# Kernel optimization log

Measured on AMD Instinct MI355X. Metric: run time of the kernel, lower is better.

## Reference

```python
import jax, jax.numpy as jnp
import numpy as np

L = 28          # num_hidden_layers (kv_cache leading dim = 2*L = 56)
H = 1024        # hidden_size
NH = 8          # num_attention_heads
KVH = 4         # num_key_value_heads
HD = 128        # head_dim
I = 3072        # mlp intermediate size
VC = 4096       # codec vocab size
NCG = 16        # num_code_groups
B = 4
S = 512         # cached seq len
THETA = 1000000.0
EPS = 1e-6


def rmsnorm(x, w):
    v = jnp.mean(jnp.square(x.astype(jnp.float32)), axis=-1, keepdims=True)
    return (x * jax.lax.rsqrt(v + EPS)).astype(x.dtype) * w


def rotate_half(x):
    h = x.shape[-1] // 2
    return jnp.concatenate([-x[..., h:], x[..., :h]], axis=-1)


def setup_inputs() -> dict:
    key = jax.random.key(0)
    ks = jax.random.split(key, 16)
    def f(k, shp, s=0.02):
        return jax.random.normal(k, shp, jnp.float32) * s
    return {
        "cb0_id": jax.random.randint(ks[0], (B, 1), 0, VC),
        "cb1_15_ids": jax.random.randint(ks[1], (B, NCG - 1), 0, VC),
        "trailing_text_embed": f(ks[2], (B, 1, H), 1.0),
        "kv_cache": f(ks[3], (2 * L, B, KVH, S, HD), 1.0),
        "position": jnp.full((B,), S, dtype=jnp.int32),
        "cb0_emb": f(ks[4], (VC, H), 1.0),
        "cp_emb": f(ks[5], (NCG - 1, VC, H), 1.0),
        "Wq": f(ks[6], (L, H, NH * HD)),
        "Wk": f(ks[7], (L, H, KVH * HD)),
        "Wv": f(ks[8], (L, H, KVH * HD)),
        "Wo": f(ks[9], (L, NH * HD, H)),
        "q_norm_w": jnp.ones((L, HD), jnp.float32),
        "k_norm_w": jnp.ones((L, HD), jnp.float32),
        "ln1_w": jnp.ones((L, H), jnp.float32),
        "ln2_w": jnp.ones((L, H), jnp.float32),
        "Wgate": f(ks[10], (L, H, I)),
        "Wup": f(ks[11], (L, H, I)),
        "Wdown": f(ks[12], (L, I, H)),
        "norm_w": jnp.ones((H,), jnp.float32),
        "head_w": f(ks[13], (H, VC)),
    }


def reference(cb0_id, cb1_15_ids, trailing_text_embed, kv_cache, position,
              cb0_emb, cp_emb, Wq, Wk, Wv, Wo, q_norm_w, k_norm_w,
              ln1_w, ln2_w, Wgate, Wup, Wdown, norm_w, head_w):
    n_rep = NH // KVH
    scale = 1.0 / np.sqrt(HD).astype(np.float32)

    # --- codebook embedding sum ---
    e = cb0_emb[cb0_id[:, 0]]                                   # [B,H]
    cp = cp_emb[jnp.arange(NCG - 1)[None, :], cb1_15_ids]       # [B,15,H]
    h = (e + cp.sum(axis=1))[:, None, :] + trailing_text_embed  # [B,1,H]

    # --- rotary at current position; broadcast shape [B,1,1,HD] ---
    inv_freq = 1.0 / (THETA ** (jnp.arange(0, HD, 2, dtype=jnp.float32) / HD))
    freqs = position.astype(jnp.float32)[:, None] * inv_freq[None, :]  # [B,HD/2]
    emb = jnp.concatenate([freqs, freqs], axis=-1)              # [B,HD]
    cos = jnp.cos(emb)[:, None, None, :]
    sin = jnp.sin(emb)[:, None, None, :]

    kv = kv_cache.reshape(L, 2, B, KVH, S, HD)

    def layer(hs, xs):
        wq, wk, wv, wo, qn, kn, l1, l2, wg, wu, wd, kc, vc = xs
        x = rmsnorm(hs, l1)
        q = (x @ wq).reshape(B, 1, NH, HD)
        k = (x @ wk).reshape(B, 1, KVH, HD)
        v = (x @ wv).reshape(B, 1, KVH, HD)
        q = jnp.transpose(rmsnorm(q, qn), (0, 2, 1, 3))   # [B,NH,1,HD]
        k = jnp.transpose(rmsnorm(k, kn), (0, 2, 1, 3))   # [B,KVH,1,HD]
        v = jnp.transpose(v, (0, 2, 1, 3))
        q = q * cos + rotate_half(q) * sin
        k = k * cos + rotate_half(k) * sin
        fk = jnp.concatenate([kc, k], axis=2)             # [B,KVH,S+1,HD]
        fv = jnp.concatenate([vc, v], axis=2)
        # GQA: head h attends kv head h // n_rep == reshape grouping (q_len = 1)
        qg = q.reshape(B, KVH, n_rep, HD)
        scores = jnp.einsum('bgrd,bgsd->bgrs', qg, fk) * scale
        w = jax.nn.softmax(scores.astype(jnp.float32), axis=-1).astype(q.dtype)
        o = jnp.einsum('bgrs,bgsd->bgrd', w, fv).reshape(B, 1, NH * HD)
        hs = hs + o @ wo
        x = rmsnorm(hs, l2)
        hs = hs + (jax.nn.silu(x @ wg) * (x @ wu)) @ wd
        return hs, (k, v)

    xs = (Wq, Wk, Wv, Wo, q_norm_w, k_norm_w, ln1_w, ln2_w,
          Wgate, Wup, Wdown, kv[:, 0], kv[:, 1])
    h, (new_k, new_v) = jax.lax.scan(layer, h, xs)

    h = rmsnorm(h, norm_w)
    past_hidden = h                                       # [B,1,H]
    logits = (h @ head_w)[:, 0, :]                        # [B,VC]

    full_k = jnp.concatenate([kv[:, 0], new_k], axis=3)   # [L,B,KVH,S+1,HD]
    full_v = jnp.concatenate([kv[:, 1], new_v], axis=3)
    new_kv_cache = jnp.stack([full_k, full_v], axis=1).reshape(2 * L, B, KVH, S + 1, HD)
    return logits, new_kv_cache, past_hidden
```

## Files before the change

kernel.cpp:

```cpp
#include <hip/hip_runtime.h>
#include <math.h>

#define L_  28
#define H_  1024
#define NH_ 8
#define KVH_ 4
#define HD_ 128
#define I_  3072
#define VC_ 4096
#define B_  4
#define S_  512
#define EPS_ 1e-6f

#define WS_H     0
#define WS_SSQ1  4096
#define WS_SSQ2  4128
#define WS_QKVP  4160
#define WS_ATTO  266304
#define WS_ATML  331840
#define WS_OPP   332864
#define WS_GUP   463936
#define WS_DWP   1250368
#define WS_HDP   1446976

__device__ __forceinline__ float wave_reduce_sum(float v) {
    #pragma unroll
    for (int off = 32; off; off >>= 1) v += __shfl_down(v, off);
    return v;
}
__device__ __forceinline__ float wave_reduce_max(float v) {
    #pragma unroll
    for (int off = 32; off; off >>= 1) v = fmaxf(v, __shfl_down(v, off));
    return v;
}

__global__ __launch_bounds__(128) void k_embed(
    const int* __restrict__ cb0, const int* __restrict__ cb1,
    const float* __restrict__ trail, const float* __restrict__ cb0e,
    const float* __restrict__ cpe, float* __restrict__ h,
    float* __restrict__ ssq1)
{
    __shared__ float red[2];
    const int t = threadIdx.x;
    const int b = blockIdx.x >> 3, sl = blockIdx.x & 7;
    const int i = sl * 128 + t;
    float v = cb0e[(size_t)cb0[b] * 1024 + i] + trail[b * 1024 + i];
    #pragma unroll
    for (int j = 0; j < 15; j++)
        v += cpe[((size_t)j * 4096 + cb1[b * 15 + j]) * 1024 + i];
    h[b * 1024 + i] = v;
    float s = wave_reduce_sum(v * v);
    if ((t & 63) == 0) red[t >> 6] = s;
    __syncthreads();
    if (t == 0) ssq1[sl * 4 + b] = red[0] + red[1];
}

template<int P>
__global__ __launch_bounds__(256) void k_norm(
    const float* __restrict__ part, float* __restrict__ h,
    float* __restrict__ ssqp)
{
    __shared__ float red[2][128];
    __shared__ float r2[2];
    const int t = threadIdx.x;
    const int b = blockIdx.x >> 3, sl = blockIdx.x & 7;
    const int col = sl * 128 + (t & 127), half = t >> 7;
    float acc = 0.f;
    #pragma unroll 8
    for (int c = half * (P / 2); c < (half + 1) * (P / 2); c++)
        acc += part[(size_t)(c * 4 + b) * 1024 + col];
    red[half][t & 127] = acc;
    __syncthreads();
    if (half == 0) {
        float v = h[b * 1024 + col] + red[0][t] + red[1][t];
        h[b * 1024 + col] = v;
        float s = wave_reduce_sum(v * v);
        if ((t & 63) == 0) r2[t >> 6] = s;
    }
    __syncthreads();
    if (t == 0) ssqp[sl * 4 + b] = r2[0] + r2[1];
}

template<int RPW, int NTOT, typename F>
__device__ __forceinline__ void gemv_core(
    const float* __restrict__ W, int ldw, int wcol0, int k0,
    float* __restrict__ xsl, float4* __restrict__ accbuf,
    float* __restrict__ pp, int colblk, int ks, F&& prologue)
{
    const int t = threadIdx.x;
    const int wv = t >> 6, lane = t & 63;
    const float* Wp = W + (size_t)(k0 + wv * RPW) * ldw + wcol0 + lane * 4;
    float4 wreg[RPW];
    #pragma unroll
    for (int i = 0; i < RPW; i++) wreg[i] = *(const float4*)(Wp + (size_t)i * ldw);
    prologue();
    const float4* xs4 = (const float4*)xsl;
    float4 a0 = {0,0,0,0}, a1 = {0,0,0,0}, a2 = {0,0,0,0}, a3 = {0,0,0,0};
    #pragma unroll
    for (int i = 0; i < RPW; i++) {
        float4 w4 = wreg[i];
        float4 xb = xs4[wv * RPW + i];
        a0.x += w4.x * xb.x; a0.y += w4.y * xb.x; a0.z += w4.z * xb.x; a0.w += w4.w * xb.x;
        a1.x += w4.x * xb.y; a1.y += w4.y * xb.y; a1.z += w4.z * xb.y; a1.w += w4.w * xb.y;
        a2.x += w4.x * xb.z; a2.y += w4.y * xb.z; a2.z += w4.z * xb.z; a2.w += w4.w * xb.z;
        a3.x += w4.x * xb.w; a3.y += w4.y * xb.w; a3.z += w4.z * xb.w; a3.w += w4.w * xb.w;
    }
    accbuf[(wv * 64 + lane) * 4 + 0] = a0;
    accbuf[(wv * 64 + lane) * 4 + 1] = a1;
    accbuf[(wv * 64 + lane) * 4 + 2] = a2;
    accbuf[(wv * 64 + lane) * 4 + 3] = a3;
    __syncthreads();
    const int l2 = t >> 2, b2 = t & 3;
    float4 s0 = accbuf[(0 * 64 + l2) * 4 + b2];
    float4 s1 = accbuf[(1 * 64 + l2) * 4 + b2];
    float4 s2 = accbuf[(2 * 64 + l2) * 4 + b2];
    float4 s3 = accbuf[(3 * 64 + l2) * 4 + b2];
    float4 s;
    s.x = s0.x + s1.x + s2.x + s3.x;
    s.y = s0.y + s1.y + s2.y + s3.y;
    s.z = s0.z + s1.z + s2.z + s3.z;
    s.w = s0.w + s1.w + s2.w + s3.w;
    *(float4*)(pp + ((size_t)ks * 4 + b2) * NTOT + colblk * 256 + l2 * 4) = s;
}

__global__ __launch_bounds__(256) void k_qkv(
    const float* __restrict__ h, const float* __restrict__ ssq1,
    const float* __restrict__ ln1,
    const float* __restrict__ Wq, const float* __restrict__ Wk,
    const float* __restrict__ Wv, float* __restrict__ qkvp)
{
    __shared__ float xsl[128];
    __shared__ float4 accbuf[1024];
    const int t = threadIdx.x;
    const int ks = blockIdx.y, k0 = ks * 32, cb = blockIdx.x;
    const float* W; int ldw, wcol0;
    if (cb < 4)      { W = Wq; ldw = 1024; wcol0 = cb * 256; }
    else if (cb < 6) { W = Wk; ldw = 512;  wcol0 = (cb - 4) * 256; }
    else             { W = Wv; ldw = 512;  wcol0 = (cb - 6) * 256; }
    gemv_core<8, 2048>(W, ldw, wcol0, k0, xsl, accbuf, qkvp, cb, ks, [&]() {
        if (t < 128) {
            const int kk = t & 31, b = t >> 5;
            float ssq = 0.f;
            #pragma unroll
            for (int i = 0; i < 8; i++) ssq += ssq1[i * 4 + b];
            const float rms = rsqrtf(ssq * (1.f / 1024.f) + EPS_);
            xsl[kk * 4 + b] = h[b * 1024 + k0 + kk] * rms * ln1[k0 + kk];
        }
        __syncthreads();
    });
}

__global__ __launch_bounds__(256) void k_attn(
    const float* __restrict__ qkvp,
    const float* __restrict__ qnw, const float* __restrict__ knw,
    const float* __restrict__ kin, const float* __restrict__ vin,
    float* __restrict__ kout, float* __restrict__ vout,
    const int* __restrict__ pos,
    float* __restrict__ opart, float* __restrict__ mlpart)
{
    __shared__ float Kl[33][129];
    __shared__ float Vl[33][129];
    __shared__ float ql[2][128];
    __shared__ float sc[2][36];
    __shared__ float red[8];

    const int t = threadIdx.x;
    const int bg = blockIdx.x, b = bg >> 2, g = bg & 3;
    const int c = blockIdx.y;
    const int lane = t & 63;
    const int r = t >> 7, d = t & 127;
    const float scale = 0.088388347648318447f;

    const float posf = (float)pos[b];
    const int j = d & 63;
    const float invf = exp2f(-(float)j * 0.31143075889569021f);
    const float ang = posf * invf;
    const float cs = cosf(ang), sn = sinf(ang);
    const int pd = (d < 64) ? d + 64 : d - 64;

    float qraw = 0.f;
    {
        const int n = (2 * g + r) * 128 + d;
        #pragma unroll
        for (int cc = 0; cc < 32; cc++) qraw += qkvp[((size_t)cc * 4 + b) * 2048 + n];
    }
    ql[r][d] = qraw;
    float ssq = wave_reduce_sum(qraw * qraw);
    if (lane == 0) red[t >> 6] = ssq;
    __syncthreads();
    const float rms_q = rsqrtf((red[r * 2] + red[r * 2 + 1]) * (1.f / 128.f) + EPS_);
    float qv = qraw * rms_q * qnw[d];
    float qp = ql[r][pd] * rms_q * qnw[pd];
    float qro = qv * cs + ((d < 64) ? -qp : qp) * sn;

    float kvraw = 0.f;
    if (c == 15) {
        const int base = (t < 128) ? (1024 + g * 128 + d) : (1536 + g * 128 + d);
        #pragma unroll
        for (int cc = 0; cc < 32; cc++) kvraw += qkvp[((size_t)cc * 4 + b) * 2048 + base];
    }
    float kss = wave_reduce_sum((t < 128) ? kvraw * kvraw : 0.f);
    __syncthreads();
    ql[r][d] = qro;
    if (lane == 0 && t < 128) red[t >> 6] = kss;
    if (c == 15) { if (t < 128) Kl[32][d] = kvraw; else Vl[32][d] = kvraw; }
    __syncthreads();
    float newkv = 0.f;
    if (c == 15) {
        if (t < 128) {
            const float rms_k = rsqrtf((red[0] + red[1]) * (1.f / 128.f) + EPS_);
            float kv_ = Kl[32][d] * rms_k * knw[d];
            float kp  = Kl[32][pd] * rms_k * knw[pd];
            newkv = kv_ * cs + ((d < 64) ? -kp : kp) * sn;
        } else {
            newkv = Vl[32][d];
        }
    }
    __syncthreads();
    const size_t out_bg = (size_t)bg * (513 * 128);
    if (c == 15) {
        if (t < 128) { Kl[32][d] = newkv; kout[out_bg + 512 * 128 + d] = newkv; }
        else         { Vl[32][d] = newkv; vout[out_bg + 512 * 128 + d] = newkv; }
    }

    const size_t in_bg = (size_t)bg * (512 * 128);
    const int s0 = c * 32;
    #pragma unroll
    for (int i = 0; i < 4; i++) {
        int f4 = i * 256 + t;
        int row = f4 >> 5, d0 = (f4 & 31) * 4;
        float4 k4 = *(const float4*)(kin + in_bg + (size_t)(s0 + row) * 128 + d0);
        float4 v4 = *(const float4*)(vin + in_bg + (size_t)(s0 + row) * 128 + d0);
        Kl[row][d0] = k4.x; Kl[row][d0 + 1] = k4.y; Kl[row][d0 + 2] = k4.z; Kl[row][d0 + 3] = k4.w;
        Vl[row][d0] = v4.x; Vl[row][d0 + 1] = v4.y; Vl[row][d0 + 2] = v4.z; Vl[row][d0 + 3] = v4.w;
        *(float4*)(kout + out_bg + (size_t)(s0 + row) * 128 + d0) = k4;
        *(float4*)(vout + out_bg + (size_t)(s0 + row) * 128 + d0) = v4;
    }
    __syncthreads();

    const int nk = (c == 15) ? 33 : 32;
    const int si = d;
    float sv = -1e30f;
    if (si < nk) {
        float a = 0.f;
        #pragma unroll 8
        for (int dd = 0; dd < 128; dd++) a += ql[r][dd] * Kl[si][dd];
        sv = a * scale;
    }
    float mv = wave_reduce_max(sv);
    if (lane == 0) red[t >> 6] = mv;
    __syncthreads();
    const float m = fmaxf(red[r * 2], red[r * 2 + 1]);
    float p = (si < nk) ? expf(sv - m) : 0.f;
    if (si < nk) sc[r][si] = p;
    float lsum = wave_reduce_sum(p);
    __syncthreads();
    if (lane == 0) red[t >> 6] = lsum;
    __syncthreads();
    const float lr = red[r * 2] + red[r * 2 + 1];
    if (d == 0) {
        mlpart[(size_t)((bg * 2 + r) * 16 + c) * 2 + 0] = m;
        mlpart[(size_t)((bg * 2 + r) * 16 + c) * 2 + 1] = lr;
    }
    float o = 0.f;
    for (int s2 = 0; s2 < nk; s2++) o += sc[r][s2] * Vl[s2][d];
    opart[(size_t)((bg * 2 + r) * 16 + c) * 128 + d] = o;
}

__global__ __launch_bounds__(256) void k_oproj(
    const float* __restrict__ atto, const float* __restrict__ atml,
    const float* __restrict__ Wo_l, float* __restrict__ opp)
{
    __shared__ float xsl[128];
    __shared__ float4 accbuf[1024];
    const int t = threadIdx.x;
    const int ks = blockIdx.y, k0 = ks * 32, cb = blockIdx.x;
    gemv_core<8, 1024>(Wo_l, 1024, cb * 256, k0, xsl, accbuf, opp, cb, ks, [&]() {
        if (t < 128) {
            const int kk = t & 31, b = t >> 5;
            const int nrow = k0 + kk;
            const int head = nrow >> 7, dh = nrow & 127;
            const int g = head >> 1, rr = head & 1;
            const size_t base = (size_t)((b * 4 + g) * 2 + rr) * 16;
            float mc[16], lc[16], M = -1e30f;
            #pragma unroll
            for (int cc = 0; cc < 16; cc++) {
                mc[cc] = atml[(base + cc) * 2];
                lc[cc] = atml[(base + cc) * 2 + 1];
                M = fmaxf(M, mc[cc]);
            }
            float Ls = 0.f, o = 0.f;
            #pragma unroll
            for (int cc = 0; cc < 16; cc++) {
                float wch = expf(mc[cc] - M);
                Ls += lc[cc] * wch;
                o += atto[(base + cc) * 128 + dh] * wch;
            }
            xsl[kk * 4 + b] = o / Ls;
        }
        __syncthreads();
    });
}

__global__ __launch_bounds__(256) void k_gateup(
    const float* __restrict__ h, const float* __restrict__ ssq2,
    const float* __restrict__ ln2,
    const float* __restrict__ Wg_l, const float* __restrict__ Wu_l,
    float* __restrict__ gup)
{
    __shared__ float xsl[128];
    __shared__ float4 accbuf[1024];
    const int t = threadIdx.x;
    const int ks = blockIdx.y, k0 = ks * 32, cb = blockIdx.x;
    const float* W; int wcol0;
    if (cb < 12) { W = Wg_l; wcol0 = cb * 256; }
    else         { W = Wu_l; wcol0 = (cb - 12) * 256; }
    gemv_core<8, 6144>(W, 3072, wcol0, k0, xsl, accbuf, gup, cb, ks, [&]() {
        if (t < 128) {
            const int kk = t & 31, b = t >> 5;
            float ssq = 0.f;
            #pragma unroll
            for (int i = 0; i < 8; i++) ssq += ssq2[i * 4 + b];
            const float rms = rsqrtf(ssq * (1.f / 1024.f) + EPS_);
            xsl[kk * 4 + b] = h[b * 1024 + k0 + kk] * rms * ln2[k0 + kk];
        }
        __syncthreads();
    });
}

__global__ __launch_bounds__(256) void k_down(
    const float* __restrict__ gup, const float* __restrict__ Wd_l,
    float* __restrict__ dwp)
{
    __shared__ float xsl[256];
    __shared__ float4 accbuf[1024];
    const int t = threadIdx.x;
    const int ks = blockIdx.y, k0 = ks * 64, cb = blockIdx.x;
    gemv_core<16, 1024>(Wd_l, 1024, cb * 256, k0, xsl, accbuf, dwp, cb, ks, [&]() {
        const int b = t >> 6, kk = t & 63;
        float gg = 0.f, uu = 0.f;
        #pragma unroll 8
        for (int cc = 0; cc < 32; cc++) {
            gg += gup[((size_t)cc * 4 + b) * 6144 + k0 + kk];
            uu += gup[((size_t)cc * 4 + b) * 6144 + 3072 + k0 + kk];
        }
        xsl[kk * 4 + b] = gg / (1.f + expf(-gg)) * uu;
        __syncthreads();
    });
}

__global__ __launch_bounds__(256) void k_head(
    const float* __restrict__ h, const float* __restrict__ ssq1,
    const float* __restrict__ normw, const float* __restrict__ headw,
    float* __restrict__ hdp, float* __restrict__ past)
{
    __shared__ float xsl[128];
    __shared__ float4 accbuf[1024];
    const int t = threadIdx.x;
    const int ks = blockIdx.y, k0 = ks * 32, cb = blockIdx.x;
    gemv_core<8, 4096>(headw, 4096, cb * 256, k0, xsl, accbuf, hdp, cb, ks, [&]() {
        if (t < 128) {
            const int kk = t & 31, b = t >> 5;
            float ssq = 0.f;
            #pragma unroll
            for (int i = 0; i < 8; i++) ssq += ssq1[i * 4 + b];
            const float rms = rsqrtf(ssq * (1.f / 1024.f) + EPS_);
            float x = h[b * 1024 + k0 + kk] * rms * normw[k0 + kk];
            xsl[kk * 4 + b] = x;
            if (cb == 0) past[b * 1024 + k0 + kk] = x;
        }
        __syncthreads();
    });
}

__global__ __launch_bounds__(256) void k_logits(
    const float* __restrict__ hdp, float* __restrict__ logits)
{
    int t4 = blockIdx.x * 256 + threadIdx.x;
    int b = t4 >> 10, n4 = t4 & 1023;
    float4 s = {0.f, 0.f, 0.f, 0.f};
    #pragma unroll
    for (int c = 0; c < 32; c++) {
        float4 v = *(const float4*)(hdp + ((size_t)c * 4 + b) * 4096 + n4 * 4);
        s.x += v.x; s.y += v.y; s.z += v.z; s.w += v.w;
    }
    *(float4*)(logits + (size_t)b * 4096 + n4 * 4) = s;
}

extern "C" void kernel_launch(void* const* d_in, const int* in_sizes, int n_in,
                              void* d_out, int out_size, void* d_ws, size_t ws_size,
                              hipStream_t stream)
{
    const int*   cb0   = (const int*)d_in[0];
    const int*   cb1   = (const int*)d_in[1];
    const float* trail = (const float*)d_in[2];
    const float* kvin  = (const float*)d_in[3];
    const int*   pos   = (const int*)d_in[4];
    const float* cb0e  = (const float*)d_in[5];
    const float* cpe   = (const float*)d_in[6];
    const float* Wq    = (const float*)d_in[7];
    const float* Wk    = (const float*)d_in[8];
    const float* Wv    = (const float*)d_in[9];
    const float* Wo    = (const float*)d_in[10];
    const float* qnw   = (const float*)d_in[11];
    const float* knw   = (const float*)d_in[12];
    const float* ln1   = (const float*)d_in[13];
    const float* ln2   = (const float*)d_in[14];
    const float* Wg    = (const float*)d_in[15];
    const float* Wu    = (const float*)d_in[16];
    const float* Wd    = (const float*)d_in[17];
    const float* normw = (const float*)d_in[18];
    const float* headw = (const float*)d_in[19];

    float* out    = (float*)d_out;
    float* logits = out;
    float* kvout  = out + 16384;
    float* past   = out + 16384 + (size_t)2 * L_ * B_ * KVH_ * (S_ + 1) * HD_;
    float* ws = (float*)d_ws;

    float* h    = ws + WS_H;
    float* ssq1 = ws + WS_SSQ1;
    float* ssq2 = ws + WS_SSQ2;
    float* qkvp = ws + WS_QKVP;
    float* atto = ws + WS_ATTO;
    float* atml = ws + WS_ATML;
    float* opp  = ws + WS_OPP;
    float* gup  = ws + WS_GUP;
    float* dwp  = ws + WS_DWP;
    float* hdp  = ws + WS_HDP;

    const size_t IN_PLANE  = (size_t)B_ * KVH_ * S_ * HD_;
    const size_t OUT_PLANE = (size_t)B_ * KVH_ * (S_ + 1) * HD_;

    k_embed<<<32, 128, 0, stream>>>(cb0, cb1, trail, cb0e, cpe, h, ssq1);

    for (int l = 0; l < L_; l++) {
        k_qkv<<<dim3(8, 32), 256, 0, stream>>>(
            h, ssq1, ln1 + (size_t)l * H_,
            Wq + (size_t)l * H_ * 1024, Wk + (size_t)l * H_ * 512,
            Wv + (size_t)l * H_ * 512, qkvp);
        k_attn<<<dim3(16, 16), 256, 0, stream>>>(
            qkvp, qnw + (size_t)l * HD_, knw + (size_t)l * HD_,
            kvin + (size_t)(2 * l) * IN_PLANE, kvin + (size_t)(2 * l + 1) * IN_PLANE,
            kvout + (size_t)(2 * l) * OUT_PLANE, kvout + (size_t)(2 * l + 1) * OUT_PLANE,
            pos, atto, atml);
        k_oproj<<<dim3(4, 32), 256, 0, stream>>>(
            atto, atml, Wo + (size_t)l * 1024 * H_, opp);
        k_norm<32><<<32, 256, 0, stream>>>(opp, h, ssq2);
        k_gateup<<<dim3(24, 32), 256, 0, stream>>>(
            h, ssq2, ln2 + (size_t)l * H_,
            Wg + (size_t)l * H_ * I_, Wu + (size_t)l * H_ * I_, gup);
        k_down<<<dim3(4, 48), 256, 0, stream>>>(
            gup, Wd + (size_t)l * I_ * H_, dwp);
        k_norm<48><<<32, 256, 0, stream>>>(dwp, h, ssq1);
    }
    k_head<<<dim3(16, 32), 256, 0, stream>>>(h, ssq1, normw, headw, hdp, past);
    k_logits<<<16, 256, 0, stream>>>(hdp, logits);
}
```

Before: 1.124 ms.

## Fuse residual reduction and RMSNorm into consumer GEMV prologues, defer RMS scaling

Removes the two standalone k_norm kernels per layer. Their work moves into the next GEMV's prologue: each block sums the residual partials for its rows and writes per-slice sum-of-squares. The per-row RMS factor is no longer applied to the GEMV input. It is applied after the GEMV instead, since it is a scalar per batch row: on V in attention, on gate/up in k_down, and on logits and past_hidden in k_logits. Q and K skip it because their per-head RMSNorm cancels it up to eps. This saves 56 launches and their serialization bubbles, at the cost of redundant partial-sum reads across column blocks and slight numeric differences from eps in the q/k norm.

```diff
diff --git a/kernel.cpp b/kernel.cpp
--- a/kernel.cpp
+++ b/kernel.cpp
@@ -12,16 +12,19 @@
 #define S_  512
 #define EPS_ 1e-6f
 
-#define WS_H     0
-#define WS_SSQ1  4096
-#define WS_SSQ2  4128
-#define WS_QKVP  4160
-#define WS_ATTO  266304
-#define WS_ATML  331840
-#define WS_OPP   332864
-#define WS_GUP   463936
-#define WS_DWP   1250368
-#define WS_HDP   1446976
+#define WS_HA    0
+#define WS_HB    4096
+#define WS_XFU   8192
+#define WS_SSQ1  12288
+#define WS_SSQ2  12416
+#define WS_SSQF  12544
+#define WS_QKVP  12672
+#define WS_ATTO  274816
+#define WS_ATML  340352
+#define WS_OPP   341376
+#define WS_GUP   472448
+#define WS_DWP   1258880
+#define WS_HDP   1455488
 
 __device__ __forceinline__ float wave_reduce_sum(float v) {
     #pragma unroll
@@ -37,10 +40,8 @@
 __global__ __launch_bounds__(128) void k_embed(
     const int* __restrict__ cb0, const int* __restrict__ cb1,
     const float* __restrict__ trail, const float* __restrict__ cb0e,
-    const float* __restrict__ cpe, float* __restrict__ h,
-    float* __restrict__ ssq1)
-{
-    __shared__ float red[2];
+    const float* __restrict__ cpe, float* __restrict__ h)
+{
     const int t = threadIdx.x;
     const int b = blockIdx.x >> 3, sl = blockIdx.x & 7;
     const int i = sl * 128 + t;
@@ -49,36 +50,6 @@
     for (int j = 0; j < 15; j++)
         v += cpe[((size_t)j * 4096 + cb1[b * 15 + j]) * 1024 + i];
     h[b * 1024 + i] = v;
-    float s = wave_reduce_sum(v * v);
-    if ((t & 63) == 0) red[t >> 6] = s;
-    __syncthreads();
-    if (t == 0) ssq1[sl * 4 + b] = red[0] + red[1];
-}
-
-template<int P>
-__global__ __launch_bounds__(256) void k_norm(
-    const float* __restrict__ part, float* __restrict__ h,
-    float* __restrict__ ssqp)
-{
-    __shared__ float red[2][128];
-    __shared__ float r2[2];
-    const int t = threadIdx.x;
-    const int b = blockIdx.x >> 3, sl = blockIdx.x & 7;
-    const int col = sl * 128 + (t & 127), half = t >> 7;
-    float acc = 0.f;
-    #pragma unroll 8
-    for (int c = half * (P / 2); c < (half + 1) * (P / 2); c++)
-        acc += part[(size_t)(c * 4 + b) * 1024 + col];
-    red[half][t & 127] = acc;
-    __syncthreads();
-    if (half == 0) {
-        float v = h[b * 1024 + col] + red[0][t] + red[1][t];
-        h[b * 1024 + col] = v;
-        float s = wave_reduce_sum(v * v);
-        if ((t & 63) == 0) r2[t >> 6] = s;
-    }
-    __syncthreads();
-    if (t == 0) ssqp[sl * 4 + b] = r2[0] + r2[1];
 }
 
 template<int RPW, int NTOT, typename F>
@@ -123,14 +94,17 @@
     *(float4*)(pp + ((size_t)ks * 4 + b2) * NTOT + colblk * 256 + l2 * 4) = s;
 }
 
+template<bool FIRST>
 __global__ __launch_bounds__(256) void k_qkv(
-    const float* __restrict__ h, const float* __restrict__ ssq1,
+    const float* __restrict__ hPrev, const float* __restrict__ dwp,
     const float* __restrict__ ln1,
     const float* __restrict__ Wq, const float* __restrict__ Wk,
-    const float* __restrict__ Wv, float* __restrict__ qkvp)
+    const float* __restrict__ Wv,
+    float* __restrict__ hA, float* __restrict__ ssqp1, float* __restrict__ qkvp)
 {
     __shared__ float xsl[128];
     __shared__ float4 accbuf[1024];
+    __shared__ float sred[128];
     const int t = threadIdx.x;
     const int ks = blockIdx.y, k0 = ks * 32, cb = blockIdx.x;
     const float* W; int ldw, wcol0;
@@ -139,19 +113,29 @@
     else             { W = Wv; ldw = 512;  wcol0 = (cb - 6) * 256; }
     gemv_core<8, 2048>(W, ldw, wcol0, k0, xsl, accbuf, qkvp, cb, ks, [&]() {
         if (t < 128) {
-            const int kk = t & 31, b = t >> 5;
-            float ssq = 0.f;
+            const int row = t >> 2, b = t & 3;
+            const int gr = k0 + row;
+            float hn = hPrev[b * 1024 + gr];
+            if (!FIRST) {
+                #pragma unroll 16
+                for (int c = 0; c < 48; c++) hn += dwp[(size_t)(c * 4 + b) * 1024 + gr];
+            }
+            sred[t] = hn * hn;
+            xsl[row * 4 + b] = hn * ln1[gr];
+            if (cb == 0) hA[b * 1024 + gr] = hn;
+        }
+        __syncthreads();
+        if (cb == 0 && t < 4) {
+            float s = 0.f;
             #pragma unroll
-            for (int i = 0; i < 8; i++) ssq += ssq1[i * 4 + b];
-            const float rms = rsqrtf(ssq * (1.f / 1024.f) + EPS_);
-            xsl[kk * 4 + b] = h[b * 1024 + k0 + kk] * rms * ln1[k0 + kk];
-        }
-        __syncthreads();
+            for (int r = 0; r < 32; r++) s += sred[r * 4 + t];
+            ssqp1[ks * 4 + t] = s;
+        }
     });
 }
 
 __global__ __launch_bounds__(256) void k_attn(
-    const float* __restrict__ qkvp,
+    const float* __restrict__ qkvp, const float* __restrict__ ssqp1,
     const float* __restrict__ qnw, const float* __restrict__ knw,
     const float* __restrict__ kin, const float* __restrict__ vin,
     float* __restrict__ kout, float* __restrict__ vout,
@@ -163,6 +147,7 @@
     __shared__ float ql[2][128];
     __shared__ float sc[2][36];
     __shared__ float red[8];
+    __shared__ float rms1sh;
 
     const int t = threadIdx.x;
     const int bg = blockIdx.x, b = bg >> 2, g = bg & 3;
@@ -170,6 +155,13 @@
     const int lane = t & 63;
     const int r = t >> 7, d = t & 127;
     const float scale = 0.088388347648318447f;
+
+    if (c == 15 && t == 0) {
+        float s = 0.f;
+        #pragma unroll
+        for (int i = 0; i < 32; i++) s += ssqp1[i * 4 + b];
+        rms1sh = rsqrtf(s * (1.f / 1024.f) + EPS_);
+    }
 
     const float posf = (float)pos[b];
     const int j = d & 63;
@@ -213,7 +205,7 @@
             float kp  = Kl[32][pd] * rms_k * knw[pd];
             newkv = kv_ * cs + ((d < 64) ? -kp : kp) * sn;
         } else {
-            newkv = Vl[32][d];
+            newkv = Vl[32][d] * rms1sh;
         }
     }
     __syncthreads();
@@ -303,13 +295,14 @@
 }
 
 __global__ __launch_bounds__(256) void k_gateup(
-    const float* __restrict__ h, const float* __restrict__ ssq2,
+    const float* __restrict__ hA, const float* __restrict__ opp,
     const float* __restrict__ ln2,
     const float* __restrict__ Wg_l, const float* __restrict__ Wu_l,
-    float* __restrict__ gup)
+    float* __restrict__ hB, float* __restrict__ ssqp2, float* __restrict__ gup)
 {
     __shared__ float xsl[128];
     __shared__ float4 accbuf[1024];
+    __shared__ float sred[128];
     const int t = threadIdx.x;
     const int ks = blockIdx.y, k0 = ks * 32, cb = blockIdx.x;
     const float* W; int wcol0;
@@ -317,74 +310,121 @@
     else         { W = Wu_l; wcol0 = (cb - 12) * 256; }
     gemv_core<8, 6144>(W, 3072, wcol0, k0, xsl, accbuf, gup, cb, ks, [&]() {
         if (t < 128) {
-            const int kk = t & 31, b = t >> 5;
-            float ssq = 0.f;
+            const int row = t >> 2, b = t & 3;
+            const int gr = k0 + row;
+            float hn = hA[b * 1024 + gr];
+            #pragma unroll 16
+            for (int c = 0; c < 32; c++) hn += opp[(size_t)(c * 4 + b) * 1024 + gr];
+            sred[t] = hn * hn;
+            xsl[row * 4 + b] = hn * ln2[gr];
+            if (cb == 0) hB[b * 1024 + gr] = hn;
+        }
+        __syncthreads();
+        if (cb == 0 && t < 4) {
+            float s = 0.f;
             #pragma unroll
-            for (int i = 0; i < 8; i++) ssq += ssq2[i * 4 + b];
-            const float rms = rsqrtf(ssq * (1.f / 1024.f) + EPS_);
-            xsl[kk * 4 + b] = h[b * 1024 + k0 + kk] * rms * ln2[k0 + kk];
-        }
-        __syncthreads();
+            for (int r = 0; r < 32; r++) s += sred[r * 4 + t];
+            ssqp2[ks * 4 + t] = s;
+        }
     });
 }
 
 __global__ __launch_bounds__(256) void k_down(
-    const float* __restrict__ gup, const float* __restrict__ Wd_l,
-    float* __restrict__ dwp)
+    const float* __restrict__ gup, const float* __restrict__ ssqp2,
+    const float* __restrict__ Wd_l, float* __restrict__ dwp)
 {
     __shared__ float xsl[256];
     __shared__ float4 accbuf[1024];
+    __shared__ float rmsb[4];
     const int t = threadIdx.x;
     const int ks = blockIdx.y, k0 = ks * 64, cb = blockIdx.x;
     gemv_core<16, 1024>(Wd_l, 1024, cb * 256, k0, xsl, accbuf, dwp, cb, ks, [&]() {
+        if (t < 4) {
+            float s = 0.f;
+            #pragma unroll
+            for (int i = 0; i < 32; i++) s += ssqp2[i * 4 + t];
+            rmsb[t] = rsqrtf(s * (1.f / 1024.f) + EPS_);
+        }
+        __syncthreads();
         const int b = t >> 6, kk = t & 63;
+        const float rm = rmsb[b];
         float gg = 0.f, uu = 0.f;
         #pragma unroll 8
         for (int cc = 0; cc < 32; cc++) {
             gg += gup[((size_t)cc * 4 + b) * 6144 + k0 + kk];
             uu += gup[((size_t)cc * 4 + b) * 6144 + 3072 + k0 + kk];
         }
+        gg *= rm; uu *= rm;
         xsl[kk * 4 + b] = gg / (1.f + expf(-gg)) * uu;
         __syncthreads();
     });
 }
 
 __global__ __launch_bounds__(256) void k_head(
-    const float* __restrict__ h, const float* __restrict__ ssq1,
+    const float* __restrict__ hB, const float* __restrict__ dwp,
     const float* __restrict__ normw, const float* __restrict__ headw,
-    float* __restrict__ hdp, float* __restrict__ past)
+    float* __restrict__ xfu, float* __restrict__ ssqpF, float* __restrict__ hdp)
 {
     __shared__ float xsl[128];
     __shared__ float4 accbuf[1024];
+    __shared__ float sred[128];
     const int t = threadIdx.x;
     const int ks = blockIdx.y, k0 = ks * 32, cb = blockIdx.x;
     gemv_core<8, 4096>(headw, 4096, cb * 256, k0, xsl, accbuf, hdp, cb, ks, [&]() {
         if (t < 128) {
-            const int kk = t & 31, b = t >> 5;
-            float ssq = 0.f;
+            const int row = t >> 2, b = t & 3;
+            const int gr = k0 + row;
+            float hn = hB[b * 1024 + gr];
+            #pragma unroll 16
+            for (int c = 0; c < 48; c++) hn += dwp[(size_t)(c * 4 + b) * 1024 + gr];
+            sred[t] = hn * hn;
+            const float x = hn * normw[gr];
+            xsl[row * 4 + b] = x;
+            if (cb == 0) xfu[b * 1024 + gr] = x;
+        }
+        __syncthreads();
+        if (cb == 0 && t < 4) {
+            float s = 0.f;
             #pragma unroll
-            for (int i = 0; i < 8; i++) ssq += ssq1[i * 4 + b];
-            const float rms = rsqrtf(ssq * (1.f / 1024.f) + EPS_);
-            float x = h[b * 1024 + k0 + kk] * rms * normw[k0 + kk];
-            xsl[kk * 4 + b] = x;
-            if (cb == 0) past[b * 1024 + k0 + kk] = x;
-        }
-        __syncthreads();
+            for (int r = 0; r < 32; r++) s += sred[r * 4 + t];
+            ssqpF[ks * 4 + t] = s;
+        }
     });
 }
 
 __global__ __launch_bounds__(256) void k_logits(
-    const float* __restrict__ hdp, float* __restrict__ logits)
-{
-    int t4 = blockIdx.x * 256 + threadIdx.x;
-    int b = t4 >> 10, n4 = t4 & 1023;
+    const float* __restrict__ hdp, const float* __restrict__ ssqpF,
+    const float* __restrict__ xfu,
+    float* __restrict__ logits, float* __restrict__ past)
+{
+    __shared__ float rsh;
+    const int t = threadIdx.x, bid = blockIdx.x;
+    const int b = bid >> 2;
+    if (t == 0) {
+        float s = 0.f;
+        #pragma unroll
+        for (int i = 0; i < 32; i++) s += ssqpF[i * 4 + b];
+        rsh = rsqrtf(s * (1.f / 1024.f) + EPS_);
+    }
+    __syncthreads();
+    const float rf = rsh;
+    const int t4 = bid * 256 + t;
+    const int n4 = t4 & 1023;
     float4 s = {0.f, 0.f, 0.f, 0.f};
     #pragma unroll
     for (int c = 0; c < 32; c++) {
         float4 v = *(const float4*)(hdp + ((size_t)c * 4 + b) * 4096 + n4 * 4);
         s.x += v.x; s.y += v.y; s.z += v.z; s.w += v.w;
     }
-    *(float4*)(logits + (size_t)b * 4096 + n4 * 4) = s;
+    s.x *= rf; s.y *= rf; s.z *= rf; s.w *= rf;
+    *(float4*)(logits + (size_t)t4 * 4) = s;
+    if (t < 64) {
+        const int p = bid * 64 + t;
+        const int i4 = p & 255;
+        float4 x = *(const float4*)(xfu + b * 1024 + i4 * 4);
+        x.x *= rf; x.y *= rf; x.z *= rf; x.w *= rf;
+        *(float4*)(past + (size_t)p * 4) = x;
+    }
 }
 
 extern "C" void kernel_launch(void* const* d_in, const int* in_sizes, int n_in,
@@ -418,42 +458,49 @@
     float* past   = out + 16384 + (size_t)2 * L_ * B_ * KVH_ * (S_ + 1) * HD_;
     float* ws = (float*)d_ws;
 
-    float* h    = ws + WS_H;
-    float* ssq1 = ws + WS_SSQ1;
-    float* ssq2 = ws + WS_SSQ2;
-    float* qkvp = ws + WS_QKVP;
-    float* atto = ws + WS_ATTO;
-    float* atml = ws + WS_ATML;
-    float* opp  = ws + WS_OPP;
-    float* gup  = ws + WS_GUP;
-    float* dwp  = ws + WS_DWP;
-    float* hdp  = ws + WS_HDP;
+    float* hA    = ws + WS_HA;
+    float* hB    = ws + WS_HB;
+    float* xfu   = ws + WS_XFU;
+    float* ssqp1 = ws + WS_SSQ1;
+    float* ssqp2 = ws + WS_SSQ2;
+    float* ssqpF = ws + WS_SSQF;
+    float* qkvp  = ws + WS_QKVP;
+    float* atto  = ws + WS_ATTO;
+    float* atml  = ws + WS_ATML;
+    float* opp   = ws + WS_OPP;
+    float* gup   = ws + WS_GUP;
+    float* dwp   = ws + WS_DWP;
+    float* hdp   = ws + WS_HDP;
 
     const size_t IN_PLANE  = (size_t)B_ * KVH_ * S_ * HD_;
     const size_t OUT_PLANE = (size_t)B_ * KVH_ * (S_ + 1) * HD_;
 
-    k_embed<<<32, 128, 0, stream>>>(cb0, cb1, trail, cb0e, cpe, h, ssq1);
+    k_embed<<<32, 128, 0, stream>>>(cb0, cb1, trail, cb0e, cpe, hB);
 
     for (int l = 0; l < L_; l++) {
-        k_qkv<<<dim3(8, 32), 256, 0, stream>>>(
-            h, ssq1, ln1 + (size_t)l * H_,
-            Wq + (size_t)l * H_ * 1024, Wk + (size_t)l * H_ * 512,
-            Wv + (size_t)l * H_ * 512, qkvp);
+        if (l == 0)
+            k_qkv<true><<<dim3(8, 32), 256, 0, stream>>>(
+                hB, dwp, ln1 + (size_t)l * H_,
+                Wq + (size_t)l * H_ * 1024, Wk + (size_t)l * H_ * 512,
+                Wv + (size_t)l * H_ * 512, hA, ssqp1, qkvp);
+        else
+            k_qkv<false><<<dim3(8, 32), 256, 0, stream>>>(
+                hB, dwp, ln1 + (size_t)l * H_,
+                Wq + (size_t)l * H_ * 1024, Wk + (size_t)l * H_ * 512,
+                Wv + (size_t)l * H_ * 512, hA, ssqp1, qkvp);
         k_attn<<<dim3(16, 16), 256, 0, stream>>>(
-            qkvp, qnw + (size_t)l * HD_, knw + (size_t)l * HD_,
+            qkvp, ssqp1, qnw + (size_t)l * HD_, knw + (size_t)l * HD_,
             kvin + (size_t)(2 * l) * IN_PLANE, kvin + (size_t)(2 * l + 1) * IN_PLANE,
             kvout + (size_t)(2 * l) * OUT_PLANE, kvout + (size_t)(2 * l + 1) * OUT_PLANE,
             pos, atto, atml);
         k_oproj<<<dim3(4, 32), 256, 0, stream>>>(
             atto, atml, Wo + (size_t)l * 1024 * H_, opp);
-        k_norm<32><<<32, 256, 0, stream>>>(opp, h, ssq2);
         k_gateup<<<dim3(24, 32), 256, 0, stream>>>(
-            h, ssq2, ln2 + (size_t)l * H_,
-            Wg + (size_t)l * H_ * I_, Wu + (size_t)l * H_ * I_, gup);
+            hA, opp, ln2 + (size_t)l * H_,
+            Wg + (size_t)l * H_ * I_, Wu + (size_t)l * H_ * I_, hB, ssqp2, gup);
         k_down<<<dim3(4, 48), 256, 0, stream>>>(
-            gup, Wd + (size_t)l * I_ * H_, dwp);
-        k_norm<48><<<32, 256, 0, stream>>>(dwp, h, ssq1);
-    }
-    k_head<<<dim3(16, 32), 256, 0, stream>>>(h, ssq1, normw, headw, hdp, past);
-    k_logits<<<16, 256, 0, stream>>>(hdp, logits);
-}
+            gup, ssqp2, Wd + (size_t)l * I_ * H_, dwp);
+    }
+    k_head<<<dim3(16, 32), 256, 0, stream>>>(hB, dwp, normw, headw, xfu, ssqpF, hdp);
+    k_logits<<<16, 256, 0, stream>>>(hdp, ssqpF, xfu, logits, past);
+}
```

Result: faster. 1.097 ms (-2.4%).
